# Performance work log

Measured on AMD Instinct MI355X. Metric: run time of the kernel, lower is better.

## Reference

```python
import jax, jax.numpy as jnp
import numpy as np

B, S, D, H = 64, 32, 1024, 1024


def setup_inputs() -> dict:
    key = jax.random.key(0)
    ks = jax.random.split(key, 12)
    sd = 1.0 / np.sqrt(D)
    sh = 1.0 / np.sqrt(H)
    return {
        "local_descs_t": jax.random.normal(ks[0], (B, S, D), jnp.float32),
        "local_descs_rot": jax.random.normal(ks[1], (B, S, D), jnp.float32),
        "scene_w": jax.random.normal(ks[2], (2 * D,), jnp.float32) * sd,
        "scene_b": jax.random.normal(ks[3], (1,), jnp.float32),
        "Wt1": jax.random.normal(ks[4], (S, D, H), jnp.float32) * sd,
        "bt1": jax.random.normal(ks[5], (S, H), jnp.float32) * 0.01,
        "Wt2": jax.random.normal(ks[6], (S, H, 3), jnp.float32) * sh,
        "bt2": jax.random.normal(ks[7], (S, 3), jnp.float32) * 0.01,
        "Wr1": jax.random.normal(ks[8], (S, D, H), jnp.float32) * sd,
        "br1": jax.random.normal(ks[9], (S, H), jnp.float32) * 0.01,
        "Wr2": jax.random.normal(ks[10], (S, H, 4), jnp.float32) * sh,
        "br2": jax.random.normal(ks[11], (S, 4), jnp.float32) * 0.01,
    }


def _pose_head(g, idx, W1, b1, W2, b2):
    # g: [B, D]; gather per-sample expert weights and run 2-layer MLP (GELU, exact erf as in F.gelu)
    h = jax.nn.gelu(jnp.einsum("bd,bdh->bh", g, W1[idx]) + b1[idx], approximate=False)
    return jnp.einsum("bh,bho->bo", h, W2[idx]) + b2[idx]


def reference(local_descs_t, local_descs_rot, scene_w, scene_b,
              Wt1, bt1, Wt2, bt2, Wr1, br1, Wr2, br2):
    # scene classification: Linear(2D -> 1) over concat descriptors, log-softmax over scenes
    logits = jnp.einsum("bsd,d->bs",
                        jnp.concatenate([local_descs_t, local_descs_rot], axis=2),
                        scene_w) + scene_b  # [B, S]
    scene_log_distr = jax.nn.log_softmax(logits, axis=1)
    idx = jnp.argmax(scene_log_distr, axis=1)  # top-1 scene per sample, [B]
    # select the chosen scene's descriptor (equivalent to one-hot mask * descs, summed over scenes)
    global_desc_t = jnp.take_along_axis(local_descs_t, idx[:, None, None], axis=1)[:, 0]    # [B, D]
    global_desc_rot = jnp.take_along_axis(local_descs_rot, idx[:, None, None], axis=1)[:, 0]
    # per-sample expert head dispatch (use_prior=False)
    x_t = _pose_head(global_desc_t, idx, Wt1, bt1, Wt2, bt2)      # [B, 3]
    x_rot = _pose_head(global_desc_rot, idx, Wr1, br1, Wr2, br2)  # [B, 4]
    expected_pose = jnp.concatenate([x_t, x_rot], axis=1)          # [B, 7]
    return expected_pose, scene_log_distr
```

## Files before the change

### kernel.cpp

```cpp
#include <hip/hip_runtime.h>
#include <math.h>

#define BB 64
#define SS 32
#define DD 1024
#define HH 1024
#define NG 40
#define GG 8

__device__ __forceinline__ float gelu_exact(float x) {
    return 0.5f * x * (1.0f + erff(x * 0.7071067811865476f));
}

__device__ __forceinline__ void gload_lds16(const float* g, float* l) {
    typedef const __attribute__((address_space(1))) unsigned int GU;
    typedef __attribute__((address_space(3))) unsigned int LU;
    __builtin_amdgcn_global_load_lds((GU*)g, (LU*)l, 16, 0, 0);
}

#define WS_LOGITS 256
#define WS_GSCENE 8448
#define WS_GSAMP  8704
#define WS_PART   32768

__global__ __launch_bounds__(256) void logits_kernel(
    const float* __restrict__ descs_t, const float* __restrict__ descs_rot,
    const float* __restrict__ scene_w, float* __restrict__ logits)
{
    const int s = blockIdx.x, b = blockIdx.y;
    const int tid = threadIdx.x, lane = tid & 63, wave = tid >> 6;

    const float4* t4 = (const float4*)(descs_t  + ((size_t)b * SS + s) * DD);
    const float4* r4 = (const float4*)(descs_rot + ((size_t)b * SS + s) * DD);
    const float4* w4t = (const float4*)(scene_w);
    const float4* w4r = (const float4*)(scene_w + DD);

    float4 a = t4[tid], w = w4t[tid];
    float acc = a.x*w.x + a.y*w.y + a.z*w.z + a.w*w.w;
    float4 a2 = r4[tid], w2 = w4r[tid];
    acc += a2.x*w2.x + a2.y*w2.y + a2.z*w2.z + a2.w*w2.w;

    #pragma unroll
    for (int off = 32; off >= 1; off >>= 1) acc += __shfl_xor(acc, off, 64);

    __shared__ float red[4];
    if (lane == 0) red[wave] = acc;
    __syncthreads();
    if (tid == 0) logits[b * SS + s] = red[0] + red[1] + red[2] + red[3];
}

__global__ __launch_bounds__(64) void finalize_scene_kernel(
    const float* __restrict__ scene_b, float* __restrict__ logits,
    int* __restrict__ idx_ws, int* __restrict__ grp_scene, int* __restrict__ grp_samp,
    float* __restrict__ out)
{
    const int b = threadIdx.x;
    const float bias = scene_b[0];
    float lg[SS];
    float m = -1e30f; int am = 0;
    #pragma unroll
    for (int s = 0; s < SS; ++s) {
        lg[s] = logits[b * SS + s] + bias;
        if (lg[s] > m) { m = lg[s]; am = s; }
    }
    float sum = 0.f;
    #pragma unroll
    for (int s = 0; s < SS; ++s) sum += expf(lg[s] - m);
    const float lse = m + logf(sum);
    #pragma unroll
    for (int s = 0; s < SS; ++s) out[BB * 7 + b * SS + s] = lg[s] - lse;
    idx_ws[b] = am;

    __shared__ int sh_cnt[SS];
    __shared__ int sh_base[SS];
    __shared__ int sh_scene[NG];
    __shared__ int sh_samp[NG][GG];

    for (int i = b; i < NG; i += 64) sh_scene[i] = -1;
    for (int i = b; i < NG * GG; i += 64) ((int*)sh_samp)[i] = -1;

    int rank = 0;
    for (int s = 0; s < SS; ++s) {
        unsigned long long mk = __ballot(am == s);
        if (am == s) rank = __popcll(mk & ((1ull << b) - 1ull));
        if (b == s) sh_cnt[s] = (int)__popcll(mk);
    }
    __syncthreads();
    if (b == 0) {
        int acc = 0;
        for (int s = 0; s < SS; ++s) {
            sh_base[s] = acc;
            acc += (sh_cnt[s] + GG - 1) / GG;
        }
    }
    __syncthreads();
    {
        const int g = sh_base[am] + rank / GG;
        const int slot = rank % GG;
        sh_samp[g][slot] = b;
        if (slot == 0) sh_scene[g] = am;
    }
    __syncthreads();
    for (int i = b; i < NG; i += 64) grp_scene[i] = sh_scene[i];
    for (int i = b; i < NG * GG; i += 64) grp_samp[i] = ((int*)sh_samp)[i];
}

template<int DSPL>
__global__ __launch_bounds__(256) void layer1_kernel(
    const float* __restrict__ descs_t, const float* __restrict__ descs_rot,
    const float* __restrict__ Wt1, const float* __restrict__ Wr1,
    const int* __restrict__ grp_scene, const int* __restrict__ grp_samp,
    float* __restrict__ part)
{
    constexpr int DS  = DD / DSPL;
    constexpr int NCH = DS / 4;
    const int dsp  = blockIdx.x;
    const int g    = blockIdx.y;
    const int head = blockIdx.z;
    const int tid  = threadIdx.x;
    const int wave = tid >> 6, lane = tid & 63;

    const int s = grp_scene[g];
    if (s < 0) return;

    __shared__ int   sh_b[GG];
    __shared__ float sh_g[DS][GG];
    __shared__ float sh_w[2 * 4 * HH];

    if (tid < GG) sh_b[tid] = grp_samp[g * GG + tid];
    __syncthreads();

    const float* descs = head ? descs_rot : descs_t;
    for (int t = tid; t < GG * (DS / 4); t += 256) {
        const int p = t / (DS / 4);
        const int c = t % (DS / 4);
        const int b = sh_b[p];
        float4 v = make_float4(0.f, 0.f, 0.f, 0.f);
        if (b >= 0)
            v = ((const float4*)(descs + ((size_t)b * SS + s) * DD + dsp * DS))[c];
        sh_g[c * 4 + 0][p] = v.x;
        sh_g[c * 4 + 1][p] = v.y;
        sh_g[c * 4 + 2][p] = v.z;
        sh_g[c * 4 + 3][p] = v.w;
    }

    const float* W0 = (head ? Wr1 : Wt1)
                    + (size_t)s * DD * HH + (size_t)dsp * DS * HH;

    #define L1_STAGE(c, buf)                                                  \
        _Pragma("unroll")                                                     \
        for (int i = 0; i < 4; ++i) {                                         \
            const int k = wave * 4 + i;                                       \
            gload_lds16(W0 + (size_t)((c) * 4 + (k >> 2)) * HH                \
                           + (k & 3) * 256 + lane * 4,                        \
                        sh_w + (buf) * (4 * HH) + k * 256);                   \
        }

    float4 acc[GG];
    #pragma unroll
    for (int p = 0; p < GG; ++p) acc[p] = make_float4(0.f, 0.f, 0.f, 0.f);

    L1_STAGE(0, 0);
    __syncthreads();

    int cur = 0;
    for (int c = 0; c < NCH; ++c) {
        if (c + 1 < NCH) { L1_STAGE(c + 1, cur ^ 1); }
        const float* wb = sh_w + cur * (4 * HH);
        const int d0 = c * 4;
        #pragma unroll
        for (int r = 0; r < 4; ++r) {
            const float4 wv = *(const float4*)(wb + r * HH + (tid << 2));
            const float4 ga = *(const float4*)&sh_g[d0 + r][0];
            const float4 gb = *(const float4*)&sh_g[d0 + r][4];
            acc[0].x += ga.x*wv.x; acc[0].y += ga.x*wv.y; acc[0].z += ga.x*wv.z; acc[0].w += ga.x*wv.w;
            acc[1].x += ga.y*wv.x; acc[1].y += ga.y*wv.y; acc[1].z += ga.y*wv.z; acc[1].w += ga.y*wv.w;
            acc[2].x += ga.z*wv.x; acc[2].y += ga.z*wv.y; acc[2].z += ga.z*wv.z; acc[2].w += ga.z*wv.w;
            acc[3].x += ga.w*wv.x; acc[3].y += ga.w*wv.y; acc[3].z += ga.w*wv.z; acc[3].w += ga.w*wv.w;
            acc[4].x += gb.x*wv.x; acc[4].y += gb.x*wv.y; acc[4].z += gb.x*wv.z; acc[4].w += gb.x*wv.w;
            acc[5].x += gb.y*wv.x; acc[5].y += gb.y*wv.y; acc[5].z += gb.y*wv.z; acc[5].w += gb.y*wv.w;
            acc[6].x += gb.z*wv.x; acc[6].y += gb.z*wv.y; acc[6].z += gb.z*wv.z; acc[6].w += gb.z*wv.w;
            acc[7].x += gb.w*wv.x; acc[7].y += gb.w*wv.y; acc[7].z += gb.w*wv.z; acc[7].w += gb.w*wv.w;
        }
        __syncthreads();
        cur ^= 1;
    }
    #undef L1_STAGE

    #pragma unroll
    for (int p = 0; p < GG; ++p) {
        const int b = sh_b[p];
        if (b >= 0) {
            float* dst = part + (((size_t)(head * BB + b) * DSPL + dsp) * HH) + tid * 4;
            *(float4*)dst = acc[p];
        }
    }
}

template<int DSPL>
__global__ __launch_bounds__(256) void head_out_kernel(
    const float* __restrict__ bt1, const float* __restrict__ Wt2, const float* __restrict__ bt2,
    const float* __restrict__ br1, const float* __restrict__ Wr2, const float* __restrict__ br2,
    const int* __restrict__ idx_ws, const float* __restrict__ part,
    float* __restrict__ out)
{
    const int b   = blockIdx.x;
    const int tid = threadIdx.x;
    const int s   = idx_ws[b];

    __shared__ float sh_h[2][HH];
    __shared__ float sh_red[7][4];

    #pragma unroll
    for (int head = 0; head < 2; ++head) {
        const float* b1 = (head ? br1 : bt1) + (size_t)s * HH;
        const float* p0 = part + ((size_t)(head * BB + b) * DSPL) * HH;
        const int j = tid * 4;
        float4 a = *(const float4*)(p0 + j);
        #pragma unroll 8
        for (int dsp = 1; dsp < DSPL; ++dsp) {
            float4 q = *(const float4*)(p0 + (size_t)dsp * HH + j);
            a.x += q.x; a.y += q.y; a.z += q.z; a.w += q.w;
        }
        float4 bb = *(const float4*)(b1 + j);
        sh_h[head][j + 0] = gelu_exact(a.x + bb.x);
        sh_h[head][j + 1] = gelu_exact(a.y + bb.y);
        sh_h[head][j + 2] = gelu_exact(a.z + bb.z);
        sh_h[head][j + 3] = gelu_exact(a.w + bb.w);
    }
    __syncthreads();

    const float* wt2 = Wt2 + (size_t)s * HH * 3;
    const float* wr2 = Wr2 + (size_t)s * HH * 4;
    float pa[7] = {0.f, 0.f, 0.f, 0.f, 0.f, 0.f, 0.f};
    for (int j = tid; j < HH; j += 256) {
        float ht = sh_h[0][j];
        float hr = sh_h[1][j];
        pa[0] += ht * wt2[j * 3 + 0];
        pa[1] += ht * wt2[j * 3 + 1];
        pa[2] += ht * wt2[j * 3 + 2];
        pa[3] += hr * wr2[j * 4 + 0];
        pa[4] += hr * wr2[j * 4 + 1];
        pa[5] += hr * wr2[j * 4 + 2];
        pa[6] += hr * wr2[j * 4 + 3];
    }
    const int lane = tid & 63, wave = tid >> 6;
    #pragma unroll
    for (int o = 0; o < 7; ++o) {
        float v = pa[o];
        #pragma unroll
        for (int off = 32; off >= 1; off >>= 1) v += __shfl_xor(v, off, 64);
        if (lane == 0) sh_red[o][wave] = v;
    }
    __syncthreads();
    if (tid < 7) {
        float v = sh_red[tid][0] + sh_red[tid][1] + sh_red[tid][2] + sh_red[tid][3];
        float bias = (tid < 3) ? bt2[(size_t)s * 3 + tid] : br2[(size_t)s * 4 + (tid - 3)];
        out[b * 7 + tid] = v + bias;
    }
}

template<int DSPL>
static void launch_pipeline(const float* descs_t, const float* descs_rot,
                            const float* Wt1, const float* Wr1,
                            const float* bt1, const float* Wt2, const float* bt2,
                            const float* br1, const float* Wr2, const float* br2,
                            int* idx_ws, int* grp_scene, int* grp_samp, float* part,
                            float* out, hipStream_t stream) {
    layer1_kernel<DSPL><<<dim3(DSPL, NG, 2), dim3(256), 0, stream>>>(
        descs_t, descs_rot, Wt1, Wr1, grp_scene, grp_samp, part);
    head_out_kernel<DSPL><<<dim3(BB), dim3(256), 0, stream>>>(
        bt1, Wt2, bt2, br1, Wr2, br2, idx_ws, part, out);
}

extern "C" void kernel_launch(void* const* d_in, const int* in_sizes, int n_in,
                              void* d_out, int out_size, void* d_ws, size_t ws_size,
                              hipStream_t stream) {
    const float* descs_t   = (const float*)d_in[0];
    const float* descs_rot = (const float*)d_in[1];
    const float* scene_w   = (const float*)d_in[2];
    const float* scene_b   = (const float*)d_in[3];
    const float* Wt1 = (const float*)d_in[4];
    const float* bt1 = (const float*)d_in[5];
    const float* Wt2 = (const float*)d_in[6];
    const float* bt2 = (const float*)d_in[7];
    const float* Wr1 = (const float*)d_in[8];
    const float* br1 = (const float*)d_in[9];
    const float* Wr2 = (const float*)d_in[10];
    const float* br2 = (const float*)d_in[11];
    float* out = (float*)d_out;

    int*   idx_ws    = (int*)d_ws;
    float* logits    = (float*)((char*)d_ws + WS_LOGITS);
    int*   grp_scene = (int*)((char*)d_ws + WS_GSCENE);
    int*   grp_samp  = (int*)((char*)d_ws + WS_GSAMP);
    float* part      = (float*)((char*)d_ws + WS_PART);

    logits_kernel<<<dim3(SS, BB), dim3(256), 0, stream>>>(
        descs_t, descs_rot, scene_w, logits);
    finalize_scene_kernel<<<dim3(1), dim3(64), 0, stream>>>(
        scene_b, logits, idx_ws, grp_scene, grp_samp, out);

    const size_t need16 = (size_t)WS_PART + (size_t)2 * BB * 16 * HH * sizeof(float);
    const size_t need8  = (size_t)WS_PART + (size_t)2 * BB * 8  * HH * sizeof(float);
    if (ws_size >= need16) {
        launch_pipeline<16>(descs_t, descs_rot, Wt1, Wr1, bt1, Wt2, bt2, br1, Wr2, br2,
                            idx_ws, grp_scene, grp_samp, part, out, stream);
    } else if (ws_size >= need8) {
        launch_pipeline<8>(descs_t, descs_rot, Wt1, Wr1, bt1, Wt2, bt2, br1, Wr2, br2,
                            idx_ws, grp_scene, grp_samp, part, out, stream);
    } else {
        launch_pipeline<4>(descs_t, descs_rot, Wt1, Wr1, bt1, Wt2, bt2, br1, Wr2, br2,
                            idx_ws, grp_scene, grp_samp, part, out, stream);
    }
}
```

Measured before the change: 60.77 us.

## Use per-wave triple-buffered LDS weight staging with vmcnt waits instead of barriers

Each wave now loads only the weight columns it consumes into its own LDS slice. This removes the block-wide __syncthreads per chunk and replaces it with s_waitcnt vmcnt counters. The pipeline deepens from double to triple buffering, so two chunks stay in flight. The cost is more LDS (48KB for weights), which may reduce occupancy, and the raw vmcnt waits rely on the compiler not issuing other vector memory ops in between.

```diff
diff --git a/kernel.cpp b/kernel.cpp
--- a/kernel.cpp
+++ b/kernel.cpp
@@ -125,7 +125,7 @@
 
     __shared__ int   sh_b[GG];
     __shared__ float sh_g[DS][GG];
-    __shared__ float sh_w[2 * 4 * HH];
+    __shared__ float sh_w[4][3][4 * 256];
 
     if (tid < GG) sh_b[tid] = grp_samp[g * GG + tid];
     __syncthreads();
@@ -143,34 +143,42 @@
         sh_g[c * 4 + 2][p] = v.z;
         sh_g[c * 4 + 3][p] = v.w;
     }
-
-    const float* W0 = (head ? Wr1 : Wt1)
-                    + (size_t)s * DD * HH + (size_t)dsp * DS * HH;
+    __syncthreads();
+
+    const float* Wg = (head ? Wr1 : Wt1)
+                    + (size_t)s * DD * HH + (size_t)dsp * DS * HH
+                    + wave * 256 + lane * 4;
 
     #define L1_STAGE(c, buf)                                                  \
         _Pragma("unroll")                                                     \
-        for (int i = 0; i < 4; ++i) {                                         \
-            const int k = wave * 4 + i;                                       \
-            gload_lds16(W0 + (size_t)((c) * 4 + (k >> 2)) * HH                \
-                           + (k & 3) * 256 + lane * 4,                        \
-                        sh_w + (buf) * (4 * HH) + k * 256);                   \
-        }
+        for (int i = 0; i < 4; ++i)                                           \
+            gload_lds16(Wg + (size_t)((c) * 4 + i) * HH,                      \
+                        &sh_w[wave][buf][i * 256]);
 
     float4 acc[GG];
     #pragma unroll
     for (int p = 0; p < GG; ++p) acc[p] = make_float4(0.f, 0.f, 0.f, 0.f);
 
     L1_STAGE(0, 0);
-    __syncthreads();
-
-    int cur = 0;
+    L1_STAGE(1, 1);
+
     for (int c = 0; c < NCH; ++c) {
-        if (c + 1 < NCH) { L1_STAGE(c + 1, cur ^ 1); }
-        const float* wb = sh_w + cur * (4 * HH);
+        const int buf = c % 3;
+        if (c + 2 < NCH) {
+            L1_STAGE(c + 2, (c + 2) % 3);
+            asm volatile("s_waitcnt vmcnt(8)" ::: "memory");
+        } else if (c + 1 < NCH) {
+            asm volatile("s_waitcnt vmcnt(4)" ::: "memory");
+        } else {
+            asm volatile("s_waitcnt vmcnt(0)" ::: "memory");
+        }
+        __builtin_amdgcn_sched_barrier(0);
+
+        const float* wb = &sh_w[wave][buf][0];
         const int d0 = c * 4;
         #pragma unroll
         for (int r = 0; r < 4; ++r) {
-            const float4 wv = *(const float4*)(wb + r * HH + (tid << 2));
+            const float4 wv = *(const float4*)(wb + r * 256 + lane * 4);
             const float4 ga = *(const float4*)&sh_g[d0 + r][0];
             const float4 gb = *(const float4*)&sh_g[d0 + r][4];
             acc[0].x += ga.x*wv.x; acc[0].y += ga.x*wv.y; acc[0].z += ga.x*wv.z; acc[0].w += ga.x*wv.w;
@@ -182,8 +190,6 @@
             acc[6].x += gb.z*wv.x; acc[6].y += gb.z*wv.y; acc[6].z += gb.z*wv.z; acc[6].w += gb.z*wv.w;
             acc[7].x += gb.w*wv.x; acc[7].y += gb.w*wv.y; acc[7].z += gb.w*wv.z; acc[7].w += gb.w*wv.w;
         }
-        __syncthreads();
-        cur ^= 1;
     }
     #undef L1_STAGE
 
@@ -191,7 +197,8 @@
     for (int p = 0; p < GG; ++p) {
         const int b = sh_b[p];
         if (b >= 0) {
-            float* dst = part + (((size_t)(head * BB + b) * DSPL + dsp) * HH) + tid * 4;
+            float* dst = part + (((size_t)(head * BB + b) * DSPL + dsp) * HH)
+                       + wave * 256 + lane * 4;
             *(float4*)dst = acc[p];
         }
     }
```

New measurement: 66.23 us. 9.0% more time.
